# Optimization experiments

Measured on AMD Instinct MI355X. Metric: run time of the kernel, lower is better.

## Reference

```python
import jax, jax.numpy as jnp
import numpy as np

B_, L, D_MODEL = 2, 2048, 1024
EXPAND, D_INNER, D_STATE, DT_RANK, D_CONV = 2, 2048, 16, 64, 4
DT_MIN, DT_MAX = 0.001, 0.1


def setup_inputs() -> dict:
    key = jax.random.key(0)
    ks = jax.random.split(key, 8)
    s = lambda fan: 1.0 / np.sqrt(fan)
    # S4D-real style init for A: A = -exp(A_log), A_log = log(1..n) repeated over d_inner
    A0 = jnp.broadcast_to(jnp.arange(1, D_STATE + 1, dtype=jnp.float32), (D_INNER, D_STATE))
    return {
        "x": jax.random.normal(ks[0], (B_, L, D_MODEL), jnp.float32),
        "W_in": jax.random.normal(ks[1], (D_MODEL, 2 * D_INNER), jnp.float32) * s(D_MODEL),
        "conv_k": jax.random.normal(ks[2], (D_CONV, D_INNER // EXPAND, D_INNER), jnp.float32) * s(D_CONV * D_INNER // EXPAND),
        "conv_b": jnp.zeros((D_INNER,), jnp.float32),
        "W_x": jax.random.normal(ks[3], (D_INNER, DT_RANK + 2 * D_STATE), jnp.float32) * s(D_INNER),
        "W_dt": jax.random.normal(ks[4], (DT_RANK, D_INNER), jnp.float32) * s(DT_RANK),
        "b_dt": jnp.zeros((D_INNER,), jnp.float32),
        "A_log": jnp.log(A0),
        "D": jnp.ones((D_INNER,), jnp.float32),
        "W_out": jax.random.normal(ks[5], (D_INNER, D_MODEL), jnp.float32) * s(D_INNER),
    }


def reference(x, W_in, conv_k, conv_b, W_x, W_dt, b_dt, A_log, D, W_out):
    # in_proj -> split into ssm branch and gating residual branch
    xz = x @ W_in                                   # (b, l, 2*d_inner)
    xs, res = jnp.split(xz, 2, axis=-1)
    # causal grouped conv1d (feature_group_count = expand)
    xc = jax.lax.conv_general_dilated(
        xs, conv_k, window_strides=(1,), padding=[(D_CONV - 1, 0)],
        dimension_numbers=("NWC", "WIO", "NWC"), feature_group_count=EXPAND,
    ) + conv_b
    u = jax.nn.silu(xc)                             # (b, l, d_inner)
    # x_proj -> delta(low-rank), B, C
    dbc = u @ W_x                                   # (b, l, dt_rank + 2n)
    dt_raw = dbc[..., :DT_RANK]
    Bm = dbc[..., DT_RANK:DT_RANK + D_STATE]        # (b, l, n)
    Cm = dbc[..., DT_RANK + D_STATE:]               # (b, l, n)
    delta = jax.nn.softplus(dt_raw @ W_dt + b_dt)   # (b, l, d_inner)
    delta = jnp.clip(delta, DT_MIN, DT_MAX)
    A = -jnp.exp(A_log)                             # (d_inner, n)
    dA = jnp.exp(delta[..., None] * A)              # (b, l, d_inner, n)
    dBu = delta[..., None] * u[..., None] * Bm[:, :, None, :]  # (b, l, d_inner, n)

    def step(h, inp):
        dA_t, dBu_t, C_t = inp                      # (b,d,n),(b,d,n),(b,n)
        h = dA_t * h + dBu_t
        y_t = jnp.einsum('bdn,bn->bd', h, C_t)
        return h, y_t

    h0 = jnp.zeros((x.shape[0], D_INNER, D_STATE), dA.dtype)
    _, y = jax.lax.scan(step, h0, (dA.transpose(1, 0, 2, 3), dBu.transpose(1, 0, 2, 3), Cm.transpose(1, 0, 2)))
    y = y.transpose(1, 0, 2) + u * D                # (b, l, d_inner)
    out = (y * jax.nn.silu(res)) @ W_out            # (b, l, d_model)
    return out
```

## Files before the change

kernel.cpp:

```cpp
#include <hip/hip_runtime.h>
#include <math.h>


typedef unsigned short ushort_t;
typedef unsigned int uint_t;
typedef __bf16 bf16x8 __attribute__((ext_vector_type(8)));
typedef float floatx4 __attribute__((ext_vector_type(4)));

#define LDS_STRIDE 40

#define GLOAD16(gp, lp) \
    __builtin_amdgcn_global_load_lds((const __attribute__((address_space(1))) void*)(gp), \
                                     (__attribute__((address_space(3))) void*)(lp), 16, 0, 0)

__device__ __forceinline__ float silu_f(float x) { return x / (1.0f + __expf(-x)); }

__device__ __forceinline__ unsigned short f2bf(float f) {
    unsigned u = __float_as_uint(f);
    unsigned r = u + 0x7fffu + ((u >> 16) & 1u);
    return (unsigned short)(r >> 16);
}
__device__ __forceinline__ float bf2f(unsigned short h) {
    return __uint_as_float(((unsigned)h) << 16);
}
__device__ __forceinline__ uint_t packhl(float v) {
    const unsigned short h = f2bf(v);
    const unsigned short l = f2bf(v - bf2f(h));
    return (uint_t)h | ((uint_t)l << 16);
}
__device__ __forceinline__ float unpack_sum(uint_t pk) {
    return __uint_as_float(pk << 16) + __uint_as_float(pk & 0xffff0000u);
}
__device__ __forceinline__ void unpack8(uint4 w0, uint4 w1, uint4& H, uint4& L) {
    H.x = (w0.x & 0xffffu) | (w0.y << 16);  L.x = (w0.x >> 16) | (w0.y & 0xffff0000u);
    H.y = (w0.z & 0xffffu) | (w0.w << 16);  L.y = (w0.z >> 16) | (w0.w & 0xffff0000u);
    H.z = (w1.x & 0xffffu) | (w1.y << 16);  L.z = (w1.x >> 16) | (w1.y & 0xffff0000u);
    H.w = (w1.z & 0xffffu) | (w1.w << 16);  L.w = (w1.z >> 16) | (w1.w & 0xffff0000u);
}
__device__ __forceinline__ size_t faddr(int n, int k, int KC) {
    return ((size_t)((n >> 4) * KC + (k >> 5)) * 64 + (n & 15) + (((k >> 3) & 3) << 4)) * 8
           + (k & 7);
}

__global__ __launch_bounds__(256) void prep_all(
    const float* __restrict__ x, const float* __restrict__ W_in,
    const float* __restrict__ conv_k, const float* __restrict__ W_out,
    const float* __restrict__ W_x,
    uint_t* __restrict__ xpk,
    ushort_t* __restrict__ WinF, ushort_t* __restrict__ convkF,
    ushort_t* __restrict__ WoutF, ushort_t* __restrict__ WxF,
    ushort_t* __restrict__ XSP_h)
{
    __shared__ float ts[32][33];
    const int bid = blockIdx.x;
    const int t = threadIdx.x;
    if (bid < 4096) {
        const size_t i4 = ((size_t)bid * 256 + t) * 4;
        float4 v = *(const float4*)&x[i4];
        uint4 pk;
        pk.x = packhl(v.x); pk.y = packhl(v.y); pk.z = packhl(v.z); pk.w = packhl(v.w);
        *(uint4*)&xpk[i4] = pk;
        return;
    }
    if (bid >= 18432 && bid < 19456) {
        const int idx = (bid - 18432) * 256 + t;
        const int r = idx >> 11, k = idx & 2047;
        float v = (r < 96) ? W_x[(size_t)k * 96 + r] : 0.f;
        WxF[faddr(r, k, 64)] = f2bf(v);
        return;
    }
    if (bid >= 19456) {
        const int idx = (bid - 19456) * 256 + t;
        const int b = idx / 6144, rem = idx % 6144;
        const int lp = rem >> 11, c = rem & 2047;
        XSP_h[((size_t)b * 2051 + lp) * 2048 + c] = 0;
        return;
    }
    const float* src; int R, C, KC; ushort_t* dst; int bx, by;
    if (bid < 8192)       { src = W_in;   R = 1024; C = 4096; KC = 32;  dst = WinF;
                            int l = bid - 4096;  bx = l & 127; by = l >> 7; }
    else if (bid < 16384) { src = conv_k; R = 4096; C = 2048; KC = 128; dst = convkF;
                            int l = bid - 8192;  bx = l & 63;  by = l >> 6; }
    else                  { src = W_out;  R = 2048; C = 1024; KC = 64;  dst = WoutF;
                            int l = bid - 16384; bx = l & 31;  by = l >> 5; }
    const int tx = t & 31, ty = t >> 5;
    const int r0 = by * 32, c0 = bx * 32;
    #pragma unroll
    for (int j = 0; j < 4; ++j)
        ts[ty + j * 8][tx] = src[(size_t)(r0 + ty + j * 8) * C + c0 + tx];
    __syncthreads();
    #pragma unroll
    for (int j = 0; j < 4; ++j) {
        const int n = c0 + ty + j * 8, k = r0 + tx;
        dst[faddr(n, k, KC)] = f2bf(ts[tx][ty + j * 8]);
    }
}

template<int MODE>
__global__ __launch_bounds__(256) void gemm2(
    const uint_t* __restrict__ Apk, const ushort_t* __restrict__ Bf, int Kfull,
    float* __restrict__ Cf, ushort_t* __restrict__ Oh)
{
    __shared__ __align__(16) ushort_t As_h[128 * LDS_STRIDE];
    __shared__ __align__(16) ushort_t As_l[128 * LDS_STRIDE];
    const int t = threadIdx.x;
    int bx, by;
    if (MODE == 2) { bx = blockIdx.x; by = blockIdx.y; }
    else {
        const int lin = blockIdx.x, xcd = lin & 7, s = lin >> 3;
        bx = s >> 2;
        by = xcd * 4 + (s & 3);
    }
    const int m0 = by * 128;
    const int n0 = (MODE == 2) ? 0 : bx * 128;
    const int kbeg = (MODE == 2) ? bx * 512 : 0;
    const int kend = (MODE == 2) ? kbeg + 512 : Kfull;
    const int KC = Kfull >> 5;
    const int lane = t & 63, wave = t >> 6;
    const int wm = (wave >> 1) * 64, wn = (wave & 1) * 64;
    const int m16 = lane & 15, q = lane >> 4;
    const int n16b = (n0 + wn) >> 4;
    const int r_0 = t >> 2, cc_0 = (t & 3) * 8;
    const int r_1 = (t + 256) >> 2, cc_1 = ((t + 256) & 3) * 8;

    uint4 a00 = *(const uint4*)&Apk[(size_t)(m0 + r_0) * Kfull + kbeg + cc_0];
    uint4 a01 = *(const uint4*)&Apk[(size_t)(m0 + r_0) * Kfull + kbeg + cc_0 + 4];
    uint4 a10 = *(const uint4*)&Apk[(size_t)(m0 + r_1) * Kfull + kbeg + cc_1];
    uint4 a11 = *(const uint4*)&Apk[(size_t)(m0 + r_1) * Kfull + kbeg + cc_1 + 4];
    bf16x8 bc[4];
    {
        const int kc = kbeg >> 5;
        #pragma unroll
        for (int j = 0; j < 4; ++j)
            bc[j] = *(const bf16x8*)&Bf[(((size_t)(n16b + j) * KC + kc) * 64 + lane) * 8];
    }

    floatx4 acc[4][4];
    const floatx4 zz = {0.f, 0.f, 0.f, 0.f};
    #pragma unroll
    for (int i = 0; i < 4; ++i)
        #pragma unroll
        for (int j = 0; j < 4; ++j) acc[i][j] = zz;

    for (int k0 = kbeg; k0 < kend; k0 += 32) {
        uint4 H, L;
        unpack8(a00, a01, H, L);
        *(uint4*)&As_h[r_0 * LDS_STRIDE + cc_0] = H;
        *(uint4*)&As_l[r_0 * LDS_STRIDE + cc_0] = L;
        unpack8(a10, a11, H, L);
        *(uint4*)&As_h[r_1 * LDS_STRIDE + cc_1] = H;
        *(uint4*)&As_l[r_1 * LDS_STRIDE + cc_1] = L;
        __syncthreads();
        bf16x8 bn[4];
        if (k0 + 32 < kend) {
            const int kn = k0 + 32, kc = kn >> 5;
            a00 = *(const uint4*)&Apk[(size_t)(m0 + r_0) * Kfull + kn + cc_0];
            a01 = *(const uint4*)&Apk[(size_t)(m0 + r_0) * Kfull + kn + cc_0 + 4];
            a10 = *(const uint4*)&Apk[(size_t)(m0 + r_1) * Kfull + kn + cc_1];
            a11 = *(const uint4*)&Apk[(size_t)(m0 + r_1) * Kfull + kn + cc_1 + 4];
            #pragma unroll
            for (int j = 0; j < 4; ++j)
                bn[j] = *(const bf16x8*)&Bf[(((size_t)(n16b + j) * KC + kc) * 64 + lane) * 8];
        }
        bf16x8 ah[4], al[4];
        #pragma unroll
        for (int i = 0; i < 4; ++i) {
            const int off = (wm + i * 16 + m16) * LDS_STRIDE + q * 8;
            ah[i] = *(const bf16x8*)&As_h[off];
            al[i] = *(const bf16x8*)&As_l[off];
        }
        #pragma unroll
        for (int i = 0; i < 4; ++i)
            #pragma unroll
            for (int j = 0; j < 4; ++j) {
                acc[i][j] = __builtin_amdgcn_mfma_f32_16x16x32_bf16(ah[i], bc[j], acc[i][j], 0, 0, 0);
                acc[i][j] = __builtin_amdgcn_mfma_f32_16x16x32_bf16(al[i], bc[j], acc[i][j], 0, 0, 0);
            }
        #pragma unroll
        for (int j = 0; j < 4; ++j) bc[j] = bn[j];
        __syncthreads();
    }

    float* Cp = (MODE == 2) ? (Cf + (size_t)bx * 393216) : Cf;
    #pragma unroll
    for (int i = 0; i < 4; ++i) {
        const int row_b = m0 + wm + i * 16 + q * 4;
        #pragma unroll
        for (int j = 0; j < 4; ++j) {
            const int col = n0 + wn + j * 16 + m16;
            #pragma unroll
            for (int rr = 0; rr < 4; ++rr) {
                const int row = row_b + rr;
                const float v = acc[i][j][rr];
                if (MODE == 0) {
                    if (n0 < 2048) {
                        const int b = row >> 11, l = row & 2047;
                        Oh[((size_t)b * 2051 + l + 3) * 2048 + col] = f2bf(v);
                    } else {
                        Cp[(size_t)row * 2048 + (col - 2048)] = v;
                    }
                } else if (MODE == 1) {
                    Cp[(size_t)row * 1024 + col] = v;
                } else {
                    if (col < 96) Cp[(size_t)row * 96 + col] = v;
                }
            }
        }
    }
}

__global__ __launch_bounds__(256, 2) void conv2(
    const ushort_t* __restrict__ Xh, const ushort_t* __restrict__ Bf,
    const float* __restrict__ bias, uint_t* __restrict__ Upk)
{
    __shared__ __align__(16) ushort_t Asw[2][128 * 64];
    __shared__ __align__(16) ushort_t Bsw[2][16 * 512];
    const int t = threadIdx.x;
    const int lin = blockIdx.x, xcd = lin & 7, s = lin >> 3;
    const int sweep = s >> 5, r = s & 31;
    const int bxp = r >> 1;
    const int by = xcd * 4 + ((sweep << 1) | (r & 1));
    const int m0 = by * 128, n0 = bxp * 128;
    const int g1024 = (n0 >= 1024) ? 1024 : 0;
    const int lane = t & 63, wave = t >> 6;
    const int wm = (wave >> 1) * 64, wn = (wave & 1) * 64;
    const int m16 = lane & 15, q = lane >> 4;
    const int l8 = lane >> 3, c8 = lane & 7;
    const int cs = c8 ^ l8;
    const int n16base = n0 >> 4;
    const int Xrow0 = (m0 >> 11) * 2051 + (m0 & 2047);

    auto stage = [&](int dbuf, int ph, int Tn) {
        const int wtap = Tn >> 4;
        const int i0 = (Tn << 6) & 1023;
        const int kc = Tn * 2 + ph;
        #pragma unroll
        for (int ii = 0; ii < 2; ++ii) {
            const int rr0 = ph * 64 + wave * 16 + ii * 8;
            const size_t gidx = (size_t)(Xrow0 + rr0 + l8 + wtap) * 2048
                              + g1024 + i0 + cs * 8;
            GLOAD16(Xh + gidx, &Asw[dbuf][rr0 * 64]);
        }
        #pragma unroll
        for (int jj = 0; jj < 2; ++jj) {
            const int jn = wave * 2 + jj;
            const size_t gidx = ((size_t)(n16base + jn) * 128 + kc) * 512 + lane * 8;
            GLOAD16(Bf + gidx, &Bsw[dbuf][(ph * 8 + jn) * 512]);
        }
    };

    floatx4 acc[4][4];
    const floatx4 zz = {0.f, 0.f, 0.f, 0.f};
    #pragma unroll
    for (int i = 0; i < 4; ++i)
        #pragma unroll
        for (int j = 0; j < 4; ++j) acc[i][j] = zz;

    auto phase = [&](int dbuf, int kcL) {
        bf16x8 ah[4], bb[4];
        #pragma unroll
        for (int mi = 0; mi < 4; ++mi) {
            const int rr2 = wm + mi * 16 + m16;
            const int ch = ((kcL << 2) | q) ^ (m16 & 7);
            ah[mi] = *(const bf16x8*)&Asw[dbuf][rr2 * 64 + ch * 8];
        }
        #pragma unroll
        for (int j = 0; j < 4; ++j) {
            const int ss = (kcL << 3) + (wn >> 4) + j;
            bb[j] = *(const bf16x8*)&Bsw[dbuf][ss * 512 + lane * 8];
        }
        __builtin_amdgcn_s_setprio(1);
        #pragma unroll
        for (int mi = 0; mi < 4; ++mi)
            #pragma unroll
            for (int j = 0; j < 4; ++j)
                acc[mi][j] = __builtin_amdgcn_mfma_f32_16x16x32_bf16(ah[mi], bb[j], acc[mi][j], 0, 0, 0);
        __builtin_amdgcn_s_setprio(0);
    };

    stage(0, 0, 0);
    stage(0, 1, 0);

    int cur = 0;
    for (int T = 0; T < 64; ++T) {
        if (T < 63) {
            stage(cur ^ 1, 0, T + 1);
            asm volatile("s_waitcnt vmcnt(4)" ::: "memory");
        } else {
            asm volatile("s_waitcnt vmcnt(0)" ::: "memory");
        }
        __builtin_amdgcn_s_barrier();
        asm volatile("" ::: "memory");
        phase(cur, 0);
        asm volatile("" ::: "memory");
        __builtin_amdgcn_s_barrier();
        asm volatile("" ::: "memory");
        if (T < 63) stage(cur ^ 1, 1, T + 1);
        phase(cur, 1);
        asm volatile("" ::: "memory");
        __builtin_amdgcn_s_barrier();
        asm volatile("" ::: "memory");
        cur ^= 1;
    }

    #pragma unroll
    for (int i = 0; i < 4; ++i) {
        const int row_b = m0 + wm + i * 16 + q * 4;
        #pragma unroll
        for (int j = 0; j < 4; ++j) {
            const int col = n0 + wn + j * 16 + m16;
            const float bz = bias[col];
            #pragma unroll
            for (int rr = 0; rr < 4; ++rr) {
                const int row = row_b + rr;
                const float v = silu_f(acc[i][j][rr] + bz);
                Upk[(size_t)row * 2048 + col] = packhl(v);
            }
        }
    }
}

__global__ __launch_bounds__(256) void dbc_reduce(
    const float* __restrict__ DBCP, float* __restrict__ DBC)
{
    const int i = blockIdx.x * 256 + threadIdx.x;
    DBC[i] = (DBCP[i] + DBCP[393216 + i]) + (DBCP[786432 + i] + DBCP[1179648 + i]);
}

__global__ __launch_bounds__(256) void delta_kernel(
    const float* __restrict__ DBC, const float* __restrict__ W_dt,
    const float* __restrict__ b_dt, float* __restrict__ DELTA)
{
    const int n  = blockIdx.x * 256 + threadIdx.x;
    const int p0 = blockIdx.y * 16;
    const int t  = threadIdx.x;
    __shared__ float dt_s[16][64];
    #pragma unroll
    for (int j = 0; j < 4; ++j) {
        const int lin = j * 256 + t;
        const int r = lin >> 6, k = lin & 63;
        dt_s[r][k] = DBC[(size_t)(p0 + r) * 96 + k];
    }
    __syncthreads();
    float acc[16];
    const float bz = b_dt[n];
    #pragma unroll
    for (int r = 0; r < 16; ++r) acc[r] = bz;
    for (int k = 0; k < 64; ++k) {
        const float wv = W_dt[(size_t)k * 2048 + n];
        #pragma unroll
        for (int r = 0; r < 16; ++r) acc[r] += dt_s[r][k] * wv;
    }
    #pragma unroll
    for (int r = 0; r < 16; ++r) {
        float a = acc[r];
        float sp = (a > 20.f) ? a : log1pf(expf(a));
        sp = fminf(fmaxf(sp, 0.001f), 0.1f);
        DELTA[(size_t)(p0 + r) * 2048 + n] = sp;
    }
}

__global__ __launch_bounds__(256) void scan_p1(
    const float* __restrict__ DELTA, const uint_t* __restrict__ Upk,
    const float* __restrict__ DBC, const float* __restrict__ A_log,
    float* __restrict__ HEND, float* __restrict__ SD)
{
    const int t = threadIdx.x;
    const int d = blockIdx.x * 256 + t;
    const int c = blockIdx.y;
    const int b = blockIdx.z;
    const int p0 = b * 2048 + c * 32;
    __shared__ float Bs[32][16];
    for (int lin = t; lin < 512; lin += 256) {
        const int s = lin >> 4, n = lin & 15;
        Bs[s][n] = DBC[(size_t)(p0 + s) * 96 + 64 + n];
    }
    __syncthreads();
    float Af[16];
    *(float4*)&Af[0]  = *(const float4*)&A_log[(size_t)d * 16 + 0];
    *(float4*)&Af[4]  = *(const float4*)&A_log[(size_t)d * 16 + 4];
    *(float4*)&Af[8]  = *(const float4*)&A_log[(size_t)d * 16 + 8];
    *(float4*)&Af[12] = *(const float4*)&A_log[(size_t)d * 16 + 12];
    #pragma unroll
    for (int n = 0; n < 16; ++n) Af[n] = -__expf(Af[n]);

    float h[16] = {};
    float sd = 0.f;
    for (int s = 0; s < 32; ++s) {
        const size_t ix = (size_t)(p0 + s) * 2048 + d;
        const float dv = DELTA[ix];
        const float uv = unpack_sum(Upk[ix]);
        const float du = dv * uv;
        sd += dv;
        #pragma unroll
        for (int n = 0; n < 16; ++n)
            h[n] = __expf(dv * Af[n]) * h[n] + du * Bs[s][n];
    }
    const size_t hb = (((size_t)c * 2 + b) * 2048 + d) * 16;
    *(float4*)&HEND[hb + 0]  = *(float4*)&h[0];
    *(float4*)&HEND[hb + 4]  = *(float4*)&h[4];
    *(float4*)&HEND[hb + 8]  = *(float4*)&h[8];
    *(float4*)&HEND[hb + 12] = *(float4*)&h[12];
    SD[((size_t)c * 2 + b) * 2048 + d] = sd;
}

__global__ __launch_bounds__(256) void scan_p2(
    const float* __restrict__ HEND, const float* __restrict__ SD,
    const float* __restrict__ A_log, float* __restrict__ HINIT)
{
    const int g = blockIdx.x * 256 + threadIdx.x;
    const int n = g & 15, d = (g >> 4) & 2047, b = (g >> 15) & 1;
    const float Af = -__expf(A_log[(size_t)d * 16 + n]);
    float h = 0.f;
    #pragma unroll 8
    for (int c = 0; c < 64; ++c) {
        const size_t cb = (size_t)c * 2 + b;
        const size_t idx = (cb * 2048 + d) * 16 + n;
        HINIT[idx] = h;
        h = __expf(Af * SD[cb * 2048 + d]) * h + HEND[idx];
    }
}

__global__ __launch_bounds__(256) void scan_p3(
    const float* __restrict__ DELTA, const uint_t* __restrict__ Upk,
    const float* __restrict__ DBC, const float* __restrict__ RES,
    const float* __restrict__ A_log, const float* __restrict__ Dp,
    const float* __restrict__ HINIT, uint_t* __restrict__ Gpk)
{
    const int t = threadIdx.x;
    const int d = blockIdx.x * 256 + t;
    const int c = blockIdx.y;
    const int b = blockIdx.z;
    const int p0 = b * 2048 + c * 32;
    __shared__ float Bs[32][16];
    __shared__ float Cs[32][16];
    for (int lin = t; lin < 512; lin += 256) {
        const int s = lin >> 4, n = lin & 15;
        Bs[s][n] = DBC[(size_t)(p0 + s) * 96 + 64 + n];
        Cs[s][n] = DBC[(size_t)(p0 + s) * 96 + 80 + n];
    }
    __syncthreads();
    float Af[16];
    *(float4*)&Af[0]  = *(const float4*)&A_log[(size_t)d * 16 + 0];
    *(float4*)&Af[4]  = *(const float4*)&A_log[(size_t)d * 16 + 4];
    *(float4*)&Af[8]  = *(const float4*)&A_log[(size_t)d * 16 + 8];
    *(float4*)&Af[12] = *(const float4*)&A_log[(size_t)d * 16 + 12];
    #pragma unroll
    for (int n = 0; n < 16; ++n) Af[n] = -__expf(Af[n]);

    const size_t hb = (((size_t)c * 2 + b) * 2048 + d) * 16;
    float h[16];
    *(float4*)&h[0]  = *(const float4*)&HINIT[hb + 0];
    *(float4*)&h[4]  = *(const float4*)&HINIT[hb + 4];
    *(float4*)&h[8]  = *(const float4*)&HINIT[hb + 8];
    *(float4*)&h[12] = *(const float4*)&HINIT[hb + 12];
    const float Dd = Dp[d];

    for (int s = 0; s < 32; ++s) {
        const int p = p0 + s;
        const size_t ix = (size_t)p * 2048 + d;
        const float dv = DELTA[ix];
        const float uv = unpack_sum(Upk[ix]);
        const float du = dv * uv;
        float y = 0.f;
        #pragma unroll
        for (int n = 0; n < 16; ++n) {
            h[n] = __expf(dv * Af[n]) * h[n] + du * Bs[s][n];
            y += h[n] * Cs[s][n];
        }
        const float resv = RES[ix];
        const float gv = (y + uv * Dd) * silu_f(resv);
        Gpk[ix] = packhl(gv);
    }
}

extern "C" void kernel_launch(void* const* d_in, const int* in_sizes, int n_in,
                              void* d_out, int out_size, void* d_ws, size_t ws_size,
                              hipStream_t stream) {
    const float* x      = (const float*)d_in[0];
    const float* W_in   = (const float*)d_in[1];
    const float* conv_k = (const float*)d_in[2];
    const float* conv_b = (const float*)d_in[3];
    const float* W_x    = (const float*)d_in[4];
    const float* W_dt   = (const float*)d_in[5];
    const float* b_dt   = (const float*)d_in[6];
    const float* A_log  = (const float*)d_in[7];
    const float* Dv     = (const float*)d_in[8];
    const float* W_out  = (const float*)d_in[9];
    float* out = (float*)d_out;

    char* base = (char*)d_ws;
    float*    RES      = (float*)(base);
    uint_t*   Upk      = (uint_t*)(base + 33554432);
    float*    DELTA    = (float*)(base + 67108864);
    ushort_t* XSP_h    = (ushort_t*)(base + 100663296);
    float*    HEND     = (float*)(base + 100663296);
    uint_t*   xpk      = (uint_t*)(base + 117465088);
    ushort_t* convkF   = (ushort_t*)(base + 134242304);
    uint_t*   Gpk      = (uint_t*)(base + 117465088);
    ushort_t* WinF     = (ushort_t*)(base + 151019520);
    ushort_t* WoutF    = (ushort_t*)(base + 159408128);
    ushort_t* WxF      = (ushort_t*)(base + 163602432);
    float*    DBCP     = (float*)(base + 164126720);
    float*    DBC      = (float*)(base + 170418176);
    float*    SD       = (float*)(base + 171991040);
    float*    HINIT    = (float*)(base + 173039616);

    prep_all<<<19504, 256, 0, stream>>>(x, W_in, conv_k, W_out, W_x,
                                        xpk, WinF, convkF, WoutF, WxF, XSP_h);
    gemm2<0><<<1024, 256, 0, stream>>>(xpk, WinF, 1024, RES, XSP_h);
    conv2<<<512, 256, 0, stream>>>(XSP_h, convkF, conv_b, Upk);
    gemm2<2><<<dim3(4, 32), 256, 0, stream>>>(Upk, WxF, 2048, DBCP, nullptr);
    dbc_reduce<<<1536, 256, 0, stream>>>(DBCP, DBC);
    delta_kernel<<<dim3(8, 256), 256, 0, stream>>>(DBC, W_dt, b_dt, DELTA);
    scan_p1<<<dim3(8, 64, 2), 256, 0, stream>>>(DELTA, Upk, DBC, A_log, HEND, SD);
    scan_p2<<<256, 256, 0, stream>>>(HEND, SD, A_log, HINIT);
    scan_p3<<<dim3(8, 64, 2), 256, 0, stream>>>(DELTA, Upk, DBC, RES, A_log, Dv,
                                                HINIT, Gpk);
    gemm2<1><<<256, 256, 0, stream>>>(Gpk, WoutF, 2048, out, nullptr);
}
```

Baseline: 517.2 us.

## Split conv2 LDS tiles per k-half and prefetch fragments into registers

```diff
diff --git a/kernel.cpp b/kernel.cpp
--- a/kernel.cpp
+++ b/kernel.cpp
@@ -213,8 +213,8 @@
     const ushort_t* __restrict__ Xh, const ushort_t* __restrict__ Bf,
     const float* __restrict__ bias, uint_t* __restrict__ Upk)
 {
-    __shared__ __align__(16) ushort_t Asw[2][128 * 64];
-    __shared__ __align__(16) ushort_t Bsw[2][16 * 512];
+    __shared__ __align__(16) ushort_t Asw[2][2][128 * 32];
+    __shared__ __align__(16) ushort_t Bsw[2][2][8 * 512];
     const int t = threadIdx.x;
     const int lin = blockIdx.x, xcd = lin & 7, s = lin >> 3;
     const int sweep = s >> 5, r = s & 31;
@@ -225,27 +225,27 @@
     const int lane = t & 63, wave = t >> 6;
     const int wm = (wave >> 1) * 64, wn = (wave & 1) * 64;
     const int m16 = lane & 15, q = lane >> 4;
-    const int l8 = lane >> 3, c8 = lane & 7;
-    const int cs = c8 ^ l8;
     const int n16base = n0 >> 4;
     const int Xrow0 = (m0 >> 11) * 2051 + (m0 & 2047);
-
-    auto stage = [&](int dbuf, int ph, int Tn) {
+    const int l16 = lane >> 2;
+    const int csA = (lane & 3) ^ ((lane >> 3) & 3);
+
+    auto stageT = [&](int dbuf, int kcL, int Tn) {
         const int wtap = Tn >> 4;
-        const int i0 = (Tn << 6) & 1023;
-        const int kc = Tn * 2 + ph;
+        const int i0 = ((Tn << 6) & 1023) + kcL * 32;
+        const int kc = Tn * 2 + kcL;
         #pragma unroll
         for (int ii = 0; ii < 2; ++ii) {
-            const int rr0 = ph * 64 + wave * 16 + ii * 8;
-            const size_t gidx = (size_t)(Xrow0 + rr0 + l8 + wtap) * 2048
-                              + g1024 + i0 + cs * 8;
-            GLOAD16(Xh + gidx, &Asw[dbuf][rr0 * 64]);
+            const int r0 = wave * 32 + ii * 16;
+            const size_t gidx = (size_t)(Xrow0 + r0 + l16 + wtap) * 2048
+                              + g1024 + i0 + csA * 8;
+            GLOAD16(Xh + gidx, &Asw[dbuf][kcL][r0 * 32]);
         }
         #pragma unroll
         for (int jj = 0; jj < 2; ++jj) {
             const int jn = wave * 2 + jj;
             const size_t gidx = ((size_t)(n16base + jn) * 128 + kc) * 512 + lane * 8;
-            GLOAD16(Bf + gidx, &Bsw[dbuf][(ph * 8 + jn) * 512]);
+            GLOAD16(Bf + gidx, &Bsw[dbuf][kcL][jn * 512]);
         }
     };
 
@@ -256,19 +256,22 @@
         #pragma unroll
         for (int j = 0; j < 4; ++j) acc[i][j] = zz;
 
-    auto phase = [&](int dbuf, int kcL) {
-        bf16x8 ah[4], bb[4];
+    bf16x8 a0[4], b0[4], a1[4], b1[4];
+
+    auto readA = [&](int dbuf, int kcL, bf16x8 (&ah)[4]) {
         #pragma unroll
         for (int mi = 0; mi < 4; ++mi) {
             const int rr2 = wm + mi * 16 + m16;
-            const int ch = ((kcL << 2) | q) ^ (m16 & 7);
-            ah[mi] = *(const bf16x8*)&Asw[dbuf][rr2 * 64 + ch * 8];
-        }
-        #pragma unroll
-        for (int j = 0; j < 4; ++j) {
-            const int ss = (kcL << 3) + (wn >> 4) + j;
-            bb[j] = *(const bf16x8*)&Bsw[dbuf][ss * 512 + lane * 8];
-        }
+            const int ch = q ^ ((m16 >> 1) & 3);
+            ah[mi] = *(const bf16x8*)&Asw[dbuf][kcL][rr2 * 32 + ch * 8];
+        }
+    };
+    auto readB = [&](int dbuf, int kcL, bf16x8 (&bb)[4]) {
+        #pragma unroll
+        for (int j = 0; j < 4; ++j)
+            bb[j] = *(const bf16x8*)&Bsw[dbuf][kcL][((wn >> 4) + j) * 512 + lane * 8];
+    };
+    auto mfma16 = [&](bf16x8 (&ah)[4], bf16x8 (&bb)[4]) {
         __builtin_amdgcn_s_setprio(1);
         #pragma unroll
         for (int mi = 0; mi < 4; ++mi)
@@ -278,29 +281,36 @@
         __builtin_amdgcn_s_setprio(0);
     };
 
-    stage(0, 0, 0);
-    stage(0, 1, 0);
+    stageT(0, 0, 0);
+    stageT(0, 1, 0);
+    asm volatile("s_waitcnt vmcnt(4)" ::: "memory");
+    __builtin_amdgcn_s_barrier();
+    asm volatile("" ::: "memory");
+    readA(0, 0, a0); readB(0, 0, b0);
 
     int cur = 0;
     for (int T = 0; T < 64; ++T) {
+        const int nxt = cur ^ 1;
         if (T < 63) {
-            stage(cur ^ 1, 0, T + 1);
+            stageT(nxt, 0, T + 1);
             asm volatile("s_waitcnt vmcnt(4)" ::: "memory");
         } else {
             asm volatile("s_waitcnt vmcnt(0)" ::: "memory");
         }
         __builtin_amdgcn_s_barrier();
         asm volatile("" ::: "memory");
-        phase(cur, 0);
+        readA(cur, 1, a1); readB(cur, 1, b1);
+        mfma16(a0, b0);
+        if (T < 63) stageT(nxt, 1, T + 1);
+        mfma16(a1, b1);
         asm volatile("" ::: "memory");
-        __builtin_amdgcn_s_barrier();
-        asm volatile("" ::: "memory");
-        if (T < 63) stage(cur ^ 1, 1, T + 1);
-        phase(cur, 1);
-        asm volatile("" ::: "memory");
-        __builtin_amdgcn_s_barrier();
-        asm volatile("" ::: "memory");
-        cur ^= 1;
+        if (T < 63) {
+            asm volatile("s_waitcnt vmcnt(4)" ::: "memory");
+            __builtin_amdgcn_s_barrier();
+            asm volatile("" ::: "memory");
+            readA(nxt, 0, a0); readB(nxt, 0, b0);
+        }
+        cur = nxt;
     }
 
     #pragma unroll
```

Result: faster. 469.2 us (-9.3%).
